# Kernel tuning notes

Measured on AMD Instinct MI355X. Metric: run time of the kernel, lower is better.

The kernel has to match this reference:

```python
import jax, jax.numpy as jnp
import numpy as np

N_NODES = 50000
N_EDGES = 800000
N_HEADS = 8
MULT = 16  # multiplicity per degree
F_KEY_NFEAT = MULT * 1 + MULT * 3  # 64


def setup_inputs() -> dict:
    key = jax.random.key(0)
    ks = jax.random.split(key, 7)
    return {
        "v0": jax.random.normal(ks[0], (N_EDGES, MULT, 1), dtype=jnp.float32),
        "v1": jax.random.normal(ks[1], (N_EDGES, MULT, 3), dtype=jnp.float32),
        "k0": jax.random.normal(ks[2], (N_EDGES, MULT, 1), dtype=jnp.float32),
        "k1": jax.random.normal(ks[3], (N_EDGES, MULT, 3), dtype=jnp.float32),
        "q0": jax.random.normal(ks[4], (N_NODES, MULT, 1), dtype=jnp.float32),
        "q1": jax.random.normal(ks[5], (N_NODES, MULT, 3), dtype=jnp.float32),
        "edge_index": jax.random.randint(ks[6], (2, N_EDGES), 0, N_NODES, dtype=jnp.int32),
    }


def _fiber2head(d0, d1, n_heads):
    # [X, m, 2d+1] -> [X, H, (m/H)*(2d+1)], concat over degrees on last axis
    x0 = d0.reshape(d0.shape[0], n_heads, -1)
    x1 = d1.reshape(d1.shape[0], n_heads, -1)
    return jnp.concatenate([x0, x1], axis=-1)


def reference(v0, v1, k0, k1, q0, q1, edge_index):
    row, col = edge_index[0], edge_index[1]
    N = q0.shape[0]
    H = N_HEADS

    k = _fiber2head(k0, k1, H)          # [E, H, 8]
    q = _fiber2head(q0, q1, H)          # [N, H, 8]

    # per-edge attention logits (dot over channel dim), scaled by sqrt(f_key.n_features)
    e = (k * q[col]).sum(axis=2) / np.float32(np.sqrt(F_KEY_NFEAT))  # [E, H]
    e = jnp.exp(e)
    s = jax.ops.segment_sum(e, row, num_segments=N)  # [N, H]
    a = e / s[row]                                   # [E, H]
    attn = a[:, :, None, None]                       # [E, H, 1, 1]

    mH = MULT // H
    # degree-0 messages: [E, H, m/H, 1]
    out0 = jax.ops.segment_sum(attn * v0.reshape(-1, H, mH, 1), col, num_segments=N)
    out0 = out0.reshape(N, MULT, 1)
    # degree-1 messages: [E, H, m/H, 3]
    out1 = jax.ops.segment_sum(attn * v1.reshape(-1, H, mH, 3), col, num_segments=N)
    out1 = out1.reshape(N, MULT, 3)
    return out0, out1
```

## Files before the change

kernel.cpp:

```cpp
#include <hip/hip_runtime.h>
#include <hip/hip_fp16.h>

#define N_NODES 50000
#define N_EDGES 800000

struct alignas(16) H8 { __half h[8]; };

__global__ __launch_bounds__(256) void k_hist(const int* __restrict__ ei,
                                              int* __restrict__ cnt_r,
                                              int* __restrict__ cnt_c)
{
    int e = blockIdx.x * blockDim.x + threadIdx.x;
    if (e >= N_EDGES) return;
    atomicAdd(cnt_r + ei[e], 1);
    atomicAdd(cnt_c + ei[N_EDGES + e], 1);
}

#define SCAN_T 1024
#define SCAN_I 8
__global__ __launch_bounds__(SCAN_T) void k_scan2(int* cnt_r, int* off_r,
                                                  int* cnt_c, int* off_c)
{
    __shared__ int sm[SCAN_T];
    __shared__ int carry_s;
    const int n = N_NODES;
    for (int pass = 0; pass < 2; ++pass) {
        int* cnt = pass ? cnt_c : cnt_r;
        int* off = pass ? off_c : off_r;
        if (threadIdx.x == 0) carry_s = 0;
        __syncthreads();
        for (int base = 0; base < n; base += SCAN_T * SCAN_I) {
            int idx0 = base + threadIdx.x * SCAN_I;
            int v[SCAN_I];
            int sum = 0;
            #pragma unroll
            for (int j = 0; j < SCAN_I; ++j) {
                int i = idx0 + j;
                v[j] = (i < n) ? cnt[i] : 0;
                sum += v[j];
            }
            sm[threadIdx.x] = sum;
            __syncthreads();
            for (int d = 1; d < SCAN_T; d <<= 1) {
                int t = (threadIdx.x >= d) ? sm[threadIdx.x - d] : 0;
                __syncthreads();
                sm[threadIdx.x] += t;
                __syncthreads();
            }
            int excl_thread = sm[threadIdx.x] - sum;
            int carry = carry_s;
            int run = carry + excl_thread;
            #pragma unroll
            for (int j = 0; j < SCAN_I; ++j) {
                int i = idx0 + j;
                if (i < n) { off[i] = run; cnt[i] = run; }
                run += v[j];
            }
            __syncthreads();
            if (threadIdx.x == SCAN_T - 1) carry_s = carry + sm[threadIdx.x];
            __syncthreads();
        }
        if (threadIdx.x == 0) off[n] = carry_s;
        __syncthreads();
    }
}

__global__ __launch_bounds__(256) void k_logits_fill(
    const float* __restrict__ k0, const float* __restrict__ k1,
    const float* __restrict__ q0, const float* __restrict__ q1,
    const int* __restrict__ ei, __half* __restrict__ e_buf,
    int* __restrict__ cur_r, int* __restrict__ cur_c,
    int* __restrict__ eid_r, int* __restrict__ eid_c)
{
    int e = blockIdx.x * blockDim.x + threadIdx.x;
    if (e >= N_EDGES) return;
    int row = ei[e];
    int col = ei[N_EDGES + e];

    const float4* k0v = (const float4*)(k0 + (size_t)e   * 16);
    const float4* q0v = (const float4*)(q0 + (size_t)col * 16);
    const float4* k1v = (const float4*)(k1 + (size_t)e   * 48);
    const float4* q1v = (const float4*)(q1 + (size_t)col * 48);

    float acc[8];
    #pragma unroll
    for (int h = 0; h < 8; ++h) acc[h] = 0.f;

    #pragma unroll
    for (int i = 0; i < 4; ++i) {
        float4 kv = k0v[i];
        float4 qv = q0v[i];
        acc[(4*i+0)/2] += kv.x * qv.x;
        acc[(4*i+1)/2] += kv.y * qv.y;
        acc[(4*i+2)/2] += kv.z * qv.z;
        acc[(4*i+3)/2] += kv.w * qv.w;
    }
    #pragma unroll
    for (int j = 0; j < 12; ++j) {
        float4 kv = k1v[j];
        float4 qv = q1v[j];
        acc[(4*j+0)/6] += kv.x * qv.x;
        acc[(4*j+1)/6] += kv.y * qv.y;
        acc[(4*j+2)/6] += kv.z * qv.z;
        acc[(4*j+3)/6] += kv.w * qv.w;
    }

    H8 pack;
    #pragma unroll
    for (int h = 0; h < 8; ++h) pack.h[h] = __float2half(__expf(acc[h] * 0.125f));
    *(H8*)(e_buf + (size_t)e * 8) = pack;

    int pr = atomicAdd(cur_r + row, 1);
    eid_r[pr] = e;
    int pc = atomicAdd(cur_c + col, 1);
    eid_c[pc] = e;
}

__global__ __launch_bounds__(256) void k_s(const __half* __restrict__ e_buf,
                                           const int* __restrict__ off_r,
                                           const int* __restrict__ eid_r,
                                           float* __restrict__ s)
{
    int t = blockIdx.x * blockDim.x + threadIdx.x;
    int node = t >> 3;
    int h = t & 7;
    if (node >= N_NODES) return;
    int beg = off_r[node], end = off_r[node + 1];
    float acc = 0.f;
    for (int i = beg; i < end; ++i) {
        int eid = eid_r[i];
        acc += __half2float(e_buf[(size_t)eid * 8 + h]);
    }
    s[(size_t)node * 8 + h] = acc;
}

__global__ __launch_bounds__(256) void k_out(
    const float* __restrict__ v0, const float* __restrict__ v1,
    const int* __restrict__ ei, const __half* __restrict__ e_buf,
    const float* __restrict__ s,
    const int* __restrict__ off_c, const int* __restrict__ eid_c,
    float* __restrict__ out0, float* __restrict__ out1)
{
    int wave = (blockIdx.x * blockDim.x + threadIdx.x) >> 6;
    int lane = threadIdx.x & 63;
    if (wave >= N_NODES) return;
    int node = wave;
    bool is0 = lane < 16;
    int f1 = lane - 16;
    int head = is0 ? (lane >> 1) : (f1 / 6);

    int beg = off_c[node], end = off_c[node + 1];
    float acc = 0.f;
    for (int i = beg; i < end; ++i) {
        int eid = eid_c[i];
        int row = ei[eid];
        float ev = __half2float(e_buf[(size_t)eid * 8 + head]);
        float sv = s[(size_t)row * 8 + head];
        float a = ev / sv;
        float v = is0 ? v0[(size_t)eid * 16 + lane]
                      : v1[(size_t)eid * 48 + f1];
        acc += a * v;
    }
    if (is0) out0[(size_t)node * 16 + lane] = acc;
    else     out1[(size_t)node * 48 + f1]   = acc;
}

extern "C" void kernel_launch(void* const* d_in, const int* in_sizes, int n_in,
                              void* d_out, int out_size, void* d_ws, size_t ws_size,
                              hipStream_t stream) {
    const float* v0 = (const float*)d_in[0];
    const float* v1 = (const float*)d_in[1];
    const float* k0 = (const float*)d_in[2];
    const float* k1 = (const float*)d_in[3];
    const float* q0 = (const float*)d_in[4];
    const float* q1 = (const float*)d_in[5];
    const int*   ei = (const int*)d_in[6];

    float* out0 = (float*)d_out;
    float* out1 = out0 + (size_t)N_NODES * 16;

    char* ws = (char*)d_ws;
    float*  s     = (float*) (ws + 0);
    __half* e_buf = (__half*)(ws + 1600000);
    int*    cnt_r = (int*)   (ws + 14400000);
    int*    cnt_c = (int*)   (ws + 14600000);
    int*    off_r = (int*)   (ws + 14800000);
    int*    off_c = (int*)   (ws + 15000016);
    int*    eid_r = (int*)   (ws + 15200032);
    int*    eid_c = (int*)   (ws + 18400032);

    hipMemsetAsync(cnt_r, 0, 400000, stream);

    const int block = 256;
    const int gridE = (N_EDGES + block - 1) / block;

    k_hist<<<gridE, block, 0, stream>>>(ei, cnt_r, cnt_c);
    k_scan2<<<1, SCAN_T, 0, stream>>>(cnt_r, off_r, cnt_c, off_c);
    k_logits_fill<<<gridE, block, 0, stream>>>(k0, k1, q0, q1, ei, e_buf,
                                               cnt_r, cnt_c, eid_r, eid_c);
    k_s<<<(N_NODES * 8 + block - 1) / block, block, 0, stream>>>(e_buf, off_r, eid_r, s);
    k_out<<<(N_NODES * 64 + block - 1) / block, block, 0, stream>>>(
        v0, v1, ei, e_buf, s, off_c, eid_c, out0, out1);
}
```

Measured before the change: 824.4 us.

## Fuse histogram into logits kernel, parallelize scan, split fill, vectorize segment sum

Moves the degree-histogram atomics into the logits kernel and drops the separate histogram pass. The CSR fill goes into its own lightweight kernel that handles four edges per thread. The serial single-block scan becomes two blocks, one per index array, each thread scanning a contiguous chunk. The softmax-denominator kernel now uses one thread per node that loads all eight halves at once instead of one thread per head. This reorders the stage schedule and trades an extra launch for less serialized scan work and fewer gathers.

```diff
diff --git a/kernel.cpp b/kernel.cpp
--- a/kernel.cpp
+++ b/kernel.cpp
@@ -6,76 +6,19 @@
 
 struct alignas(16) H8 { __half h[8]; };
 
-__global__ __launch_bounds__(256) void k_hist(const int* __restrict__ ei,
-                                              int* __restrict__ cnt_r,
-                                              int* __restrict__ cnt_c)
-{
-    int e = blockIdx.x * blockDim.x + threadIdx.x;
-    if (e >= N_EDGES) return;
-    atomicAdd(cnt_r + ei[e], 1);
-    atomicAdd(cnt_c + ei[N_EDGES + e], 1);
-}
-
-#define SCAN_T 1024
-#define SCAN_I 8
-__global__ __launch_bounds__(SCAN_T) void k_scan2(int* cnt_r, int* off_r,
-                                                  int* cnt_c, int* off_c)
-{
-    __shared__ int sm[SCAN_T];
-    __shared__ int carry_s;
-    const int n = N_NODES;
-    for (int pass = 0; pass < 2; ++pass) {
-        int* cnt = pass ? cnt_c : cnt_r;
-        int* off = pass ? off_c : off_r;
-        if (threadIdx.x == 0) carry_s = 0;
-        __syncthreads();
-        for (int base = 0; base < n; base += SCAN_T * SCAN_I) {
-            int idx0 = base + threadIdx.x * SCAN_I;
-            int v[SCAN_I];
-            int sum = 0;
-            #pragma unroll
-            for (int j = 0; j < SCAN_I; ++j) {
-                int i = idx0 + j;
-                v[j] = (i < n) ? cnt[i] : 0;
-                sum += v[j];
-            }
-            sm[threadIdx.x] = sum;
-            __syncthreads();
-            for (int d = 1; d < SCAN_T; d <<= 1) {
-                int t = (threadIdx.x >= d) ? sm[threadIdx.x - d] : 0;
-                __syncthreads();
-                sm[threadIdx.x] += t;
-                __syncthreads();
-            }
-            int excl_thread = sm[threadIdx.x] - sum;
-            int carry = carry_s;
-            int run = carry + excl_thread;
-            #pragma unroll
-            for (int j = 0; j < SCAN_I; ++j) {
-                int i = idx0 + j;
-                if (i < n) { off[i] = run; cnt[i] = run; }
-                run += v[j];
-            }
-            __syncthreads();
-            if (threadIdx.x == SCAN_T - 1) carry_s = carry + sm[threadIdx.x];
-            __syncthreads();
-        }
-        if (threadIdx.x == 0) off[n] = carry_s;
-        __syncthreads();
-    }
-}
-
-__global__ __launch_bounds__(256) void k_logits_fill(
+__global__ __launch_bounds__(256) void k_logits(
     const float* __restrict__ k0, const float* __restrict__ k1,
     const float* __restrict__ q0, const float* __restrict__ q1,
     const int* __restrict__ ei, __half* __restrict__ e_buf,
-    int* __restrict__ cur_r, int* __restrict__ cur_c,
-    int* __restrict__ eid_r, int* __restrict__ eid_c)
+    int* __restrict__ cnt_r, int* __restrict__ cnt_c)
 {
     int e = blockIdx.x * blockDim.x + threadIdx.x;
     if (e >= N_EDGES) return;
     int row = ei[e];
     int col = ei[N_EDGES + e];
+
+    atomicAdd(cnt_r + row, 1);
+    atomicAdd(cnt_c + col, 1);
 
     const float4* k0v = (const float4*)(k0 + (size_t)e   * 16);
     const float4* q0v = (const float4*)(q0 + (size_t)col * 16);
@@ -109,11 +52,66 @@
     #pragma unroll
     for (int h = 0; h < 8; ++h) pack.h[h] = __float2half(__expf(acc[h] * 0.125f));
     *(H8*)(e_buf + (size_t)e * 8) = pack;
-
-    int pr = atomicAdd(cur_r + row, 1);
-    eid_r[pr] = e;
-    int pc = atomicAdd(cur_c + col, 1);
-    eid_c[pc] = e;
+}
+
+#define SCAN_T 1024
+#define SCAN_C 49
+__global__ __launch_bounds__(SCAN_T) void k_scan(int* __restrict__ cnt_r, int* __restrict__ off_r,
+                                                 int* __restrict__ cnt_c, int* __restrict__ off_c)
+{
+    __shared__ int sm[SCAN_T];
+    int* cnt = blockIdx.x ? cnt_c : cnt_r;
+    int* off = blockIdx.x ? off_c : off_r;
+    const int n = N_NODES;
+    int t = threadIdx.x;
+    int base = t * SCAN_C;
+
+    int sum = 0;
+    #pragma unroll 4
+    for (int j = 0; j < SCAN_C; ++j) {
+        int i = base + j;
+        if (i < n) sum += cnt[i];
+    }
+    sm[t] = sum;
+    __syncthreads();
+    #pragma unroll
+    for (int d = 1; d < SCAN_T; d <<= 1) {
+        int v = (t >= d) ? sm[t - d] : 0;
+        __syncthreads();
+        sm[t] += v;
+        __syncthreads();
+    }
+    int run = sm[t] - sum;
+    for (int j = 0; j < SCAN_C; ++j) {
+        int i = base + j;
+        if (i < n) {
+            int v = cnt[i];
+            off[i] = run;
+            cnt[i] = run;
+            run += v;
+        }
+    }
+    if (t == 0) off[n] = sm[SCAN_T - 1];
+}
+
+__global__ __launch_bounds__(256) void k_fill(const int* __restrict__ ei,
+                                              int* __restrict__ cur_r, int* __restrict__ cur_c,
+                                              int* __restrict__ eid_r, int* __restrict__ eid_c)
+{
+    int t = blockIdx.x * blockDim.x + threadIdx.x;
+    int e4 = t * 4;
+    if (e4 >= N_EDGES) return;
+    int4 rows = *(const int4*)(ei + e4);
+    int4 cols = *(const int4*)(ei + N_EDGES + e4);
+    int r[4] = {rows.x, rows.y, rows.z, rows.w};
+    int c[4] = {cols.x, cols.y, cols.z, cols.w};
+    #pragma unroll
+    for (int j = 0; j < 4; ++j) {
+        int pr = atomicAdd(cur_r + r[j], 1);
+        eid_r[pr] = e4 + j;
+        int pc = atomicAdd(cur_c + c[j], 1);
+        eid_c[pc] = e4 + j;
+    }
 }
 
 __global__ __launch_bounds__(256) void k_s(const __half* __restrict__ e_buf,
@@ -121,17 +119,21 @@
                                            const int* __restrict__ eid_r,
                                            float* __restrict__ s)
 {
-    int t = blockIdx.x * blockDim.x + threadIdx.x;
-    int node = t >> 3;
-    int h = t & 7;
+    int node = blockIdx.x * blockDim.x + threadIdx.x;
     if (node >= N_NODES) return;
     int beg = off_r[node], end = off_r[node + 1];
-    float acc = 0.f;
+    float acc[8];
+    #pragma unroll
+    for (int h = 0; h < 8; ++h) acc[h] = 0.f;
     for (int i = beg; i < end; ++i) {
         int eid = eid_r[i];
-        acc += __half2float(e_buf[(size_t)eid * 8 + h]);
-    }
-    s[(size_t)node * 8 + h] = acc;
+        H8 p = *(const H8*)(e_buf + (size_t)eid * 8);
+        #pragma unroll
+        for (int h = 0; h < 8; ++h) acc[h] += __half2float(p.h[h]);
+    }
+    float4* sv = (float4*)(s + (size_t)node * 8);
+    sv[0] = make_float4(acc[0], acc[1], acc[2], acc[3]);
+    sv[1] = make_float4(acc[4], acc[5], acc[6], acc[7]);
 }
 
 __global__ __launch_bounds__(256) void k_out(
@@ -194,11 +196,10 @@
     const int block = 256;
     const int gridE = (N_EDGES + block - 1) / block;
 
-    k_hist<<<gridE, block, 0, stream>>>(ei, cnt_r, cnt_c);
-    k_scan2<<<1, SCAN_T, 0, stream>>>(cnt_r, off_r, cnt_c, off_c);
-    k_logits_fill<<<gridE, block, 0, stream>>>(k0, k1, q0, q1, ei, e_buf,
-                                               cnt_r, cnt_c, eid_r, eid_c);
-    k_s<<<(N_NODES * 8 + block - 1) / block, block, 0, stream>>>(e_buf, off_r, eid_r, s);
+    k_logits<<<gridE, block, 0, stream>>>(k0, k1, q0, q1, ei, e_buf, cnt_r, cnt_c);
+    k_scan<<<2, SCAN_T, 0, stream>>>(cnt_r, off_r, cnt_c, off_c);
+    k_fill<<<(N_EDGES / 4 + block - 1) / block, block, 0, stream>>>(ei, cnt_r, cnt_c, eid_r, eid_c);
+    k_s<<<(N_NODES + block - 1) / block, block, 0, stream>>>(e_buf, off_r, eid_r, s);
     k_out<<<(N_NODES * 64 + block - 1) / block, block, 0, stream>>>(
         v0, v1, ei, e_buf, s, off_c, eid_c, out0, out1);
 }
```

After: 854.6 us. 3.7% more time.
